# Performance work log

Measured on AMD Instinct MI355X. Metric: run time of the kernel, lower is better.

## Reference

```python
import jax, jax.numpy as jnp
import numpy as np

B, NMAX, D, NUM = 1024, 128, 256, 4
EPS = 1e-8
NEG = -1e9


def segment_softmax(logits, seg):
    # torch_geometric-style softmax over ragged segments. logits: (T,)
    m = jax.ops.segment_max(logits, seg, num_segments=B)
    e = jnp.exp(logits - m[seg])
    s = jax.ops.segment_sum(e, seg, num_segments=B)
    return e / (s[seg] + 1e-16)


def to_dense(v, seg, pos):
    # scatter ragged rows into (B, NMAX, ...) dense batch
    return jnp.zeros((B, NMAX) + v.shape[1:], v.dtype).at[seg, pos].set(v)


def uot_badmm(x, q0d, maskf, a1, a2, a3, rho):
    # Bregman-ADMM solver for entropic unbalanced OT (f_method='badmm-e').
    # x: (B,N,D) cost (to be maximized); q0d, maskf: (B,N,1); a1,a2,a3,rho: (NUM,)
    log_p0 = jnp.full((B, 1, D), -jnp.log(float(D)), x.dtype)  # uniform dim prior
    log_q0 = jnp.log(q0d + EPS)                                # (B,N,1)
    log_t = log_q0 + log_p0                                    # T init = q0 p0^T
    log_s = log_t
    log_mu = log_p0
    log_eta = log_q0
    z = jnp.zeros_like(x)
    z1 = jnp.zeros_like(log_p0)
    z2 = jnp.zeros_like(log_q0)
    neg = (1.0 - maskf) * NEG  # exclude padded rows from N-axis softmax
    for k in range(NUM):
        r, b1, b2, b3 = rho[k], a1[k], a2[k], a3[k]
        # T-update: rows (over D) sum to eta
        y = (x - z + r * log_s) / (b2 + r)
        log_t = log_eta + jax.nn.log_softmax(y, axis=2)
        # S-update: columns (over N) sum to mu, masked
        y = (z + r * log_t) / (b1 + r) + neg
        log_s = log_mu + jax.nn.log_softmax(y, axis=1)
        # unbalanced marginal updates (KL to priors, weight a3)
        log_mu = (b3 * log_p0 - z1 + r * jax.nn.logsumexp(log_s, axis=1, keepdims=True)) / (b3 + r)
        log_eta = (b3 * log_q0 - z2 + r * jax.nn.logsumexp(log_t, axis=2, keepdims=True)) / (b3 + r)
        # dual ascent
        t = jnp.exp(log_t) * maskf
        s = jnp.exp(log_s) * maskf
        z = z + r * (t - s)
        z1 = z1 + r * (jnp.exp(log_mu) - jnp.sum(s, axis=1, keepdims=True))
        z2 = z2 + r * (jnp.exp(log_eta) - jnp.sum(t, axis=2, keepdims=True)) * maskf
    return jnp.exp(log_t) * maskf


def setup_inputs() -> dict:
    rng = np.random.default_rng(0)
    lengths = rng.integers(NMAX // 2, NMAX + 1, size=B)
    lengths[0] = NMAX  # ensure max size present
    batch = jnp.asarray(np.repeat(np.arange(B), lengths), dtype=jnp.int32)
    total = int(lengths.sum())
    ks = jax.random.split(jax.random.key(0), 8)
    x = jax.random.normal(ks[0], (total, D), jnp.float32)
    W1 = jax.random.normal(ks[1], (2 * D, D), jnp.float32) / np.float32(np.sqrt(D))
    W2 = jax.random.normal(ks[2], (1, 2 * D), jnp.float32) / np.float32(np.sqrt(2 * D))
    rho = 0.1 * jax.random.normal(ks[3], (NUM,), jnp.float32)
    a1 = 0.1 * jax.random.normal(ks[4], (NUM,), jnp.float32)
    a2 = 0.1 * jax.random.normal(ks[5], (NUM,), jnp.float32)
    a3 = 0.1 * jax.random.normal(ks[6], (NUM,), jnp.float32)
    return {"x": x, "batch": batch, "W1": W1, "W2": W2, "rho": rho, "a1": a1, "a2": a2, "a3": a3}


def reference(x, batch, W1, W2, rho, a1, a2, a3):
    # attention-based sample prior q0 (q0 != 'fixed' branch)
    h = jnp.tanh(x @ W1.T)          # (T, 2D)
    logits = (h @ W2.T)[:, 0]       # (T,)
    q0 = segment_softmax(logits, batch)[:, None]  # (T, 1)
    # ragged -> dense batch (to_dense_batch)
    counts = jax.ops.segment_sum(jnp.ones_like(batch), batch, num_segments=B)
    starts = jnp.cumsum(counts) - counts
    pos = jnp.arange(batch.shape[0]) - starts[batch]
    xd = to_dense(x, batch, pos)    # (B, NMAX, D)
    q0d = to_dense(q0, batch, pos)  # (B, NMAX, 1)
    mask = to_dense(jnp.ones((batch.shape[0], 1), x.dtype), batch, pos)  # (B, NMAX, 1)
    trans = uot_badmm(xd, q0d, mask,
                      jax.nn.softplus(a1), jax.nn.softplus(a2),
                      jax.nn.softplus(a3), jax.nn.softplus(rho))
    frot = D * xd * trans * mask    # (B, NMAX, D)
    return jnp.sum(frot, axis=1)    # (B, D)
```

## Files before the change

### kernel.cpp

```cpp
#include <hip/hip_runtime.h>
#include <math.h>

#define BB   1024
#define DD   256
#define LOGD 5.5451774444795624753f

typedef __attribute__((ext_vector_type(8))) short short8;
typedef __attribute__((ext_vector_type(4))) float f32x4;

__device__ __forceinline__ float wave_sum(float v){
  #pragma unroll
  for (int off=32; off>0; off>>=1) v += __shfl_xor(v, off, 64);
  return v;
}
__device__ __forceinline__ float wave_max(float v){
  #pragma unroll
  for (int off=32; off>0; off>>=1) v = fmaxf(v, __shfl_xor(v, off, 64));
  return v;
}
__device__ __forceinline__ float fast_tanh(float x){
  return 1.0f - 2.0f/(__expf(2.0f*x)+1.0f);
}
__device__ __forceinline__ unsigned short f2bf(float f){
  unsigned int u = __float_as_uint(f);
  unsigned int r = u + 0x7FFFu + ((u >> 16) & 1u);
  return (unsigned short)(r >> 16);
}

__global__ void k_pre(const float* __restrict__ W1, unsigned short* __restrict__ w1b,
                      const int* __restrict__ batch, int T, int* __restrict__ starts,
                      const float* __restrict__ rho, const float* __restrict__ a1,
                      const float* __restrict__ a2, const float* __restrict__ a3,
                      float* __restrict__ P)
{
  const int blk = blockIdx.x, tid = threadIdx.x;
  if (blk < 64){
    const int t = blk*256 + tid;
    #pragma unroll
    for (int i=0;i<2;i++){
      const int idx = (t*2 + i)*4;
      const float4 v = *(const float4*)(W1 + idx);
      *(ushort4*)(w1b + idx) = make_ushort4(f2bf(v.x), f2bf(v.y), f2bf(v.z), f2bf(v.w));
    }
  } else if (blk < 69){
    const int b = (blk-64)*256 + tid;
    if (b <= BB){
      int lo = 0, hi = T;
      while (lo < hi){ int mid = (lo+hi)>>1; if (batch[mid] < b) lo = mid+1; else hi = mid; }
      starts[b] = lo;
    }
  } else if (tid == 0){
    float lm = -LOGD, z1 = 0.f;
    for (int k=0;k<4;k++){
      float r  = log1pf(expf(rho[k]));
      float b1 = log1pf(expf(a1[k]));
      float b2 = log1pf(expf(a2[k]));
      float b3 = log1pf(expf(a3[k]));
      P[k]    = r;
      P[4+k]  = 1.f/(b1+r);
      P[8+k]  = 1.f/(b2+r);
      P[12+k] = lm;
      P[16+k] = b3;
      P[20+k] = 1.f/(b3+r);
      float lmn = (b3*(-LOGD) - z1 + r*lm)/(b3+r);
      z1 += r*(expf(lmn)-expf(lm));
      lm = lmn;
    }
  }
}

#define LPW 72
__global__ __launch_bounds__(512, 2) void k_mlp(
    const float* __restrict__ x, const unsigned short* __restrict__ w1b,
    const float* __restrict__ W2, float* __restrict__ logits, int T)
{
  __shared__ unsigned short Xs[128*LPW];
  __shared__ unsigned short Ws[128*LPW];
  __shared__ float lred[128];
  const int by = blockIdx.x;
  const int bx = blockIdx.y;
  const int tid = threadIdx.x;
  if (tid < 128) lred[tid] = 0.f;

  const int l = tid & 63;
  const int w = tid >> 6;
  const int wm = w >> 2;
  const int wn = w & 3;
  const int lr = l & 15, quad = l >> 4;
  const int srow = tid >> 2;
  const int sseg = tid & 3;
  const int wrow = tid >> 3;
  const int wseg = tid & 7;

  f32x4 acc[4][2];
  #pragma unroll
  for (int mi=0;mi<4;mi++)
    #pragma unroll
    for (int ni=0;ni<2;ni++) acc[mi][ni] = (f32x4){0.f,0.f,0.f,0.f};

  for (int kt=0; kt<4; kt++){
    const int k0 = kt*64;
    {
      const int grow = bx*128 + srow;
      #pragma unroll
      for (int i=0;i<4;i++){
        float4 v = make_float4(0.f,0.f,0.f,0.f);
        if (grow < T) v = *(const float4*)(x + (size_t)grow*DD + k0 + sseg*16 + i*4);
        *(ushort4*)&Xs[srow*LPW + sseg*16 + i*4] =
            make_ushort4(f2bf(v.x), f2bf(v.y), f2bf(v.z), f2bf(v.w));
      }
    }
    #pragma unroll
    for (int h=0; h<2; h++){
      const int r = h*64 + wrow;
      *(short8*)&Ws[r*LPW + wseg*8] =
          *(const short8*)(w1b + (size_t)(by*128 + r)*DD + k0 + wseg*8);
    }
    __syncthreads();
    #pragma unroll
    for (int ks=0; ks<2; ks++){
      short8 afr[4], bfr[2];
      #pragma unroll
      for (int mi=0;mi<4;mi++)
        afr[mi] = *(const short8*)&Xs[(wm*64 + mi*16 + lr)*LPW + ks*32 + quad*8];
      #pragma unroll
      for (int ni=0;ni<2;ni++)
        bfr[ni] = *(const short8*)&Ws[(wn*32 + ni*16 + lr)*LPW + ks*32 + quad*8];
      #pragma unroll
      for (int mi=0;mi<4;mi++)
        #pragma unroll
        for (int ni=0;ni<2;ni++)
          acc[mi][ni] = __builtin_amdgcn_mfma_f32_16x16x32_bf16(afr[mi], bfr[ni], acc[mi][ni], 0, 0, 0);
    }
    __syncthreads();
  }

  float w2v[2];
  #pragma unroll
  for (int ni=0;ni<2;ni++) w2v[ni] = W2[by*128 + wn*32 + ni*16 + lr];
  #pragma unroll
  for (int mi=0;mi<4;mi++){
    float p[4];
    #pragma unroll
    for (int v=0; v<4; v++){
      p[v] = fast_tanh(acc[mi][0][v])*w2v[0] + fast_tanh(acc[mi][1][v])*w2v[1];
      #pragma unroll
      for (int off=1; off<16; off<<=1) p[v] += __shfl_xor(p[v], off, 64);
    }
    if (lr == 0){
      #pragma unroll
      for (int v=0; v<4; v++)
        atomicAdd(&lred[wm*64 + mi*16 + quad*4 + v], p[v]);
    }
  }
  __syncthreads();
  if (tid < 128){
    const int grow = bx*128 + tid;
    if (grow < T) atomicAdd(logits + grow, lred[tid]);
  }
}

__global__ __launch_bounds__(1024, 4) void k_solver(
    const float* __restrict__ x, const float* __restrict__ logits,
    const int* __restrict__ starts, const float* __restrict__ P,
    float* __restrict__ out)
{
  __shared__ float A[128*DD];
  __shared__ float red[16*DD];
  __shared__ float colv[DD];
  const int b = blockIdx.x;
  const int start = starts[b];
  const int len = starts[b+1] - start;
  const int tid = threadIdx.x;
  const int w = tid >> 6, l = tid & 63;
  const int n0 = w*8;
  int nv = len - n0; nv = nv < 0 ? 0 : (nv > 8 ? 8 : nv);

  const float r0=P[0], r1=P[1], r2=P[2], r3=P[3];
  const float i10=P[4], i11=P[5], i12=P[6];
  const float i20=P[8], i21=P[9], i22=P[10], i23=P[11];
  const float mu0=P[12], mu1=P[13], mu2=P[14];
  const float b30=P[16], b31=P[17], b32=P[18];
  const float e30=P[20], e31=P[21], e32=P[22];

  const float* lg = logits + start;
  float v0 = (l      < len) ? lg[l]    : -3.0e38f;
  float v1 = (l+64   < len) ? lg[l+64] : -3.0e38f;
  float sm = wave_max(fmaxf(v0,v1));
  float se0 = (l    < len) ? __expf(v0-sm) : 0.f;
  float se1 = (l+64 < len) ? __expf(v1-sm) : 0.f;
  float ssum = wave_sum(se0+se1);
  const float sinv = 1.f/(ssum + 1e-16f);
  const float esel = (n0 < 64) ? se0 : se1;

  float lq[8], eta[8], z2r[8];
  float z[8][4];
  #pragma unroll
  for (int r=0;r<8;r++){
    const float ev = __shfl(esel, (n0+r)&63, 64);
    lq[r]  = __logf(ev*sinv + 1e-8f);
    eta[r] = lq[r];
    z2r[r] = 0.f;
    #pragma unroll
    for (int j=0;j<4;j++) z[r][j]=0.f;
  }

  {
    float sp[4] = {0.f,0.f,0.f,0.f};
    #pragma unroll
    for (int r=0;r<8;r++){
      if (r < nv){
        const float* xp = x + (size_t)(start+n0+r)*DD + l;
        const int base = (n0+r)*DD + l;
        const float a0 = lq[r] - LOGD;
        float xv[4], y[4];
        #pragma unroll
        for (int j=0;j<4;j++) xv[j] = xp[64*j];
        #pragma unroll
        for (int j=0;j<4;j++) y[j] = (xv[j] + r0*a0) * i20;
        float se = 0.f;
        #pragma unroll
        for (int j=0;j<4;j++) se += __expf(y[j]);
        se = wave_sum(se);
        const float off = eta[r] - __logf(se);
        #pragma unroll
        for (int j=0;j<4;j++){
          const float lt = off + y[j];
          A[base+64*j] = lt;
          sp[j] += __expf((r0*lt) * i10);
        }
        const float en = (b30*lq[r] - z2r[r] + r0*eta[r]) * e30;
        z2r[r] += r0*(__expf(en) - __expf(eta[r]));
        eta[r] = en;
      }
    }
    #pragma unroll
    for (int j=0;j<4;j++) red[w*DD + l + 64*j] = sp[j];
  }
  __syncthreads();
  if (tid < DD){
    float s = 0.f;
    #pragma unroll
    for (int ww=0; ww<16; ww++) s += red[ww*DD + tid];
    colv[tid] = __logf(s);
  }
  __syncthreads();

  #pragma unroll
  for (int k=1;k<3;k++){
    const float rkm = (k==1)? r0 : r1;
    const float ib1m= (k==1)? i10 : i11;
    const float mum = (k==1)? mu0 : mu1;
    const float rk  = (k==1)? r1 : r2;
    const float ib1k= (k==1)? i11 : i12;
    const float ib2k= (k==1)? i21 : i22;
    const float b3k = (k==1)? b31 : b32;
    const float e3k = (k==1)? e31 : e32;
    float lsc[4];
    #pragma unroll
    for (int j=0;j<4;j++) lsc[j] = colv[l+64*j];
    float sp[4] = {0.f,0.f,0.f,0.f};
    #pragma unroll
    for (int r=0;r<8;r++){
      if (r < nv){
        const float* xp = x + (size_t)(start+n0+r)*DD + l;
        const int base = (n0+r)*DD + l;
        float xv[4];
        #pragma unroll
        for (int j=0;j<4;j++) xv[j] = xp[64*j];
        float y[4], lsn[4];
        #pragma unroll
        for (int j=0;j<4;j++){
          const float lt  = A[base+64*j];
          const float ys  = (z[r][j] + rkm*lt) * ib1m;
          lsn[j] = mum + ys - lsc[j];
          z[r][j] += rkm*(__expf(lt) - __expf(lsn[j]));
          y[j] = (xv[j] - z[r][j] + rk*lsn[j]) * ib2k;
        }
        float se = 0.f;
        #pragma unroll
        for (int j=0;j<4;j++) se += __expf(y[j]);
        se = wave_sum(se);
        const float off = eta[r] - __logf(se);
        #pragma unroll
        for (int j=0;j<4;j++){
          const float lt = off + y[j];
          A[base+64*j] = lt;
          sp[j] += __expf((z[r][j] + rk*lt) * ib1k);
        }
        const float en = (b3k*lq[r] - z2r[r] + rk*eta[r]) * e3k;
        z2r[r] += rk*(__expf(en) - __expf(eta[r]));
        eta[r] = en;
      }
    }
    #pragma unroll
    for (int j=0;j<4;j++) red[w*DD + l + 64*j] = sp[j];
    __syncthreads();
    if (tid < DD){
      float s = 0.f;
      #pragma unroll
      for (int ww=0; ww<16; ww++) s += red[ww*DD + tid];
      colv[tid] = __logf(s);
    }
    __syncthreads();
  }

  {
    float lsc[4];
    #pragma unroll
    for (int j=0;j<4;j++) lsc[j] = colv[l+64*j];
    float op[4] = {0.f,0.f,0.f,0.f};
    #pragma unroll
    for (int r=0;r<8;r++){
      if (r < nv){
        const float* xp = x + (size_t)(start+n0+r)*DD + l;
        const int base = (n0+r)*DD + l;
        float xv[4];
        #pragma unroll
        for (int j=0;j<4;j++) xv[j] = xp[64*j];
        float y[4];
        #pragma unroll
        for (int j=0;j<4;j++){
          const float lt  = A[base+64*j];
          const float ys  = (z[r][j] + r2*lt) * i12;
          const float lsn = mu2 + ys - lsc[j];
          z[r][j] += r2*(__expf(lt) - __expf(lsn));
          y[j] = (xv[j] - z[r][j] + r3*lsn) * i23;
        }
        float ey[4], se = 0.f;
        #pragma unroll
        for (int j=0;j<4;j++){ ey[j] = __expf(y[j]); se += ey[j]; }
        se = wave_sum(se);
        const float rs = __expf(eta[r]) / se;
        #pragma unroll
        for (int j=0;j<4;j++) op[j] += xv[j]*ey[j]*rs;
      }
    }
    #pragma unroll
    for (int j=0;j<4;j++) red[w*DD + l + 64*j] = op[j];
    __syncthreads();
    if (tid < DD){
      float s = 0.f;
      #pragma unroll
      for (int ww=0; ww<16; ww++) s += red[ww*DD + tid];
      out[(size_t)b*DD + tid] = 256.0f * s;
    }
  }
}

extern "C" void kernel_launch(void* const* d_in, const int* in_sizes, int n_in,
                              void* d_out, int out_size, void* d_ws, size_t ws_size,
                              hipStream_t stream) {
  const float* x    = (const float*)d_in[0];
  const int*   batch= (const int*)d_in[1];
  const float* W1   = (const float*)d_in[2];
  const float* W2   = (const float*)d_in[3];
  const float* rho  = (const float*)d_in[4];
  const float* a1   = (const float*)d_in[5];
  const float* a2   = (const float*)d_in[6];
  const float* a3   = (const float*)d_in[7];
  float* out = (float*)d_out;
  const int T = in_sizes[1];

  float* logits = (float*)d_ws;
  int*   starts = (int*)(logits + T);
  float* P      = (float*)(starts + 1028);
  unsigned short* w1b = (unsigned short*)(P + 32);

  k_pre<<<70, 256, 0, stream>>>(W1, w1b, batch, T, starts, rho, a1, a2, a3, P);
  hipMemsetAsync(logits, 0, (size_t)T*sizeof(float), stream);
  k_mlp<<<dim3(4, (T+127)/128), 512, 0, stream>>>(x, w1b, W2, logits, T);
  k_solver<<<BB, 1024, 0, stream>>>(x, logits, starts, P, out);
}
```

Before: 358.2 us.

## Keep full x tile resident in MLP, drop memset, use LDS atomics in solver

The MLP kernel now loads a row tile of x once into LDS as bf16 across the full K dimension and loops over all four hidden-column chunks inside one block. Logits are written directly instead of accumulated with global atomics, so the memset launch is removed. In the solver, the 16-way shared reduction buffer plus its extra barrier pass is replaced by LDS atomicAdd into a triple-buffered column array, which saves one barrier per iteration and some LDS. The cost is larger LDS use in k_mlp (about 135 KB per block, against 36 KB before), fewer and longer MLP blocks, and contention on the shared atomics.

Result: slower. 472.4 us (+31.9%).

```diff
diff --git a/kernel.cpp b/kernel.cpp
--- a/kernel.cpp
+++ b/kernel.cpp
@@ -69,94 +69,88 @@
   }
 }
 
-#define LPW 72
+#define LPX 264
 __global__ __launch_bounds__(512, 2) void k_mlp(
     const float* __restrict__ x, const unsigned short* __restrict__ w1b,
     const float* __restrict__ W2, float* __restrict__ logits, int T)
 {
-  __shared__ unsigned short Xs[128*LPW];
-  __shared__ unsigned short Ws[128*LPW];
+  __shared__ unsigned short Xs[128*LPX];
+  __shared__ unsigned short Ws[128*LPX];
   __shared__ float lred[128];
-  const int by = blockIdx.x;
-  const int bx = blockIdx.y;
+  const int bx = blockIdx.x;
   const int tid = threadIdx.x;
   if (tid < 128) lred[tid] = 0.f;
+
+  const int srow = tid >> 2, sseg = tid & 3;
+  {
+    const int grow = bx*128 + srow;
+    #pragma unroll
+    for (int i=0;i<16;i++){
+      float4 v = make_float4(0.f,0.f,0.f,0.f);
+      if (grow < T) v = *(const float4*)(x + (size_t)grow*DD + sseg*64 + i*4);
+      *(ushort4*)&Xs[srow*LPX + sseg*64 + i*4] =
+          make_ushort4(f2bf(v.x), f2bf(v.y), f2bf(v.z), f2bf(v.w));
+    }
+  }
 
   const int l = tid & 63;
   const int w = tid >> 6;
   const int wm = w >> 2;
   const int wn = w & 3;
   const int lr = l & 15, quad = l >> 4;
-  const int srow = tid >> 2;
-  const int sseg = tid & 3;
-  const int wrow = tid >> 3;
-  const int wseg = tid & 7;
-
-  f32x4 acc[4][2];
-  #pragma unroll
-  for (int mi=0;mi<4;mi++)
-    #pragma unroll
-    for (int ni=0;ni<2;ni++) acc[mi][ni] = (f32x4){0.f,0.f,0.f,0.f};
-
-  for (int kt=0; kt<4; kt++){
-    const int k0 = kt*64;
-    {
-      const int grow = bx*128 + srow;
-      #pragma unroll
-      for (int i=0;i<4;i++){
-        float4 v = make_float4(0.f,0.f,0.f,0.f);
-        if (grow < T) v = *(const float4*)(x + (size_t)grow*DD + k0 + sseg*16 + i*4);
-        *(ushort4*)&Xs[srow*LPW + sseg*16 + i*4] =
-            make_ushort4(f2bf(v.x), f2bf(v.y), f2bf(v.z), f2bf(v.w));
-      }
-    }
-    #pragma unroll
-    for (int h=0; h<2; h++){
-      const int r = h*64 + wrow;
-      *(short8*)&Ws[r*LPW + wseg*8] =
-          *(const short8*)(w1b + (size_t)(by*128 + r)*DD + k0 + wseg*8);
-    }
+
+  for (int hq=0; hq<4; hq++){
     __syncthreads();
     #pragma unroll
-    for (int ks=0; ks<2; ks++){
+    for (int i=0;i<8;i++){
+      *(short8*)&Ws[srow*LPX + sseg*64 + i*8] =
+          *(const short8*)(w1b + (size_t)(hq*128 + srow)*DD + sseg*64 + i*8);
+    }
+    __syncthreads();
+
+    f32x4 acc[4][2];
+    #pragma unroll
+    for (int mi=0;mi<4;mi++)
+      #pragma unroll
+      for (int ni=0;ni<2;ni++) acc[mi][ni] = (f32x4){0.f,0.f,0.f,0.f};
+    #pragma unroll
+    for (int ks=0; ks<8; ks++){
       short8 afr[4], bfr[2];
       #pragma unroll
       for (int mi=0;mi<4;mi++)
-        afr[mi] = *(const short8*)&Xs[(wm*64 + mi*16 + lr)*LPW + ks*32 + quad*8];
+        afr[mi] = *(const short8*)&Xs[(wm*64 + mi*16 + lr)*LPX + ks*32 + quad*8];
       #pragma unroll
       for (int ni=0;ni<2;ni++)
-        bfr[ni] = *(const short8*)&Ws[(wn*32 + ni*16 + lr)*LPW + ks*32 + quad*8];
+        bfr[ni] = *(const short8*)&Ws[(wn*32 + ni*16 + lr)*LPX + ks*32 + quad*8];
       #pragma unroll
       for (int mi=0;mi<4;mi++)
         #pragma unroll
         for (int ni=0;ni<2;ni++)
           acc[mi][ni] = __builtin_amdgcn_mfma_f32_16x16x32_bf16(afr[mi], bfr[ni], acc[mi][ni], 0, 0, 0);
     }
-    __syncthreads();
-  }
-
-  float w2v[2];
-  #pragma unroll
-  for (int ni=0;ni<2;ni++) w2v[ni] = W2[by*128 + wn*32 + ni*16 + lr];
-  #pragma unroll
-  for (int mi=0;mi<4;mi++){
-    float p[4];
-    #pragma unroll
-    for (int v=0; v<4; v++){
-      p[v] = fast_tanh(acc[mi][0][v])*w2v[0] + fast_tanh(acc[mi][1][v])*w2v[1];
-      #pragma unroll
-      for (int off=1; off<16; off<<=1) p[v] += __shfl_xor(p[v], off, 64);
-    }
-    if (lr == 0){
-      #pragma unroll
-      for (int v=0; v<4; v++)
-        atomicAdd(&lred[wm*64 + mi*16 + quad*4 + v], p[v]);
+    float w2v[2];
+    #pragma unroll
+    for (int ni=0;ni<2;ni++) w2v[ni] = W2[hq*128 + wn*32 + ni*16 + lr];
+    #pragma unroll
+    for (int mi=0;mi<4;mi++){
+      float p[4];
+      #pragma unroll
+      for (int v=0; v<4; v++){
+        p[v] = fast_tanh(acc[mi][0][v])*w2v[0] + fast_tanh(acc[mi][1][v])*w2v[1];
+        #pragma unroll
+        for (int off=1; off<16; off<<=1) p[v] += __shfl_xor(p[v], off, 64);
+      }
+      if (lr == 0){
+        #pragma unroll
+        for (int v=0; v<4; v++)
+          atomicAdd(&lred[wm*64 + mi*16 + quad*4 + v], p[v]);
+      }
     }
   }
   __syncthreads();
   if (tid < 128){
     const int grow = bx*128 + tid;
-    if (grow < T) atomicAdd(logits + grow, lred[tid]);
+    if (grow < T) logits[grow] = lred[tid];
   }
 }
 
@@ -166,8 +160,7 @@
     float* __restrict__ out)
 {
   __shared__ float A[128*DD];
-  __shared__ float red[16*DD];
-  __shared__ float colv[DD];
+  __shared__ float cols[3][DD];
   const int b = blockIdx.x;
   const int start = starts[b];
   const int len = starts[b+1] - start;
@@ -204,6 +197,8 @@
     #pragma unroll
     for (int j=0;j<4;j++) z[r][j]=0.f;
   }
+  if (tid < DD){ cols[0][tid] = 0.f; cols[1][tid] = 0.f; }
+  __syncthreads();
 
   {
     float sp[4] = {0.f,0.f,0.f,0.f};
@@ -234,15 +229,10 @@
         eta[r] = en;
       }
     }
-    #pragma unroll
-    for (int j=0;j<4;j++) red[w*DD + l + 64*j] = sp[j];
-  }
-  __syncthreads();
-  if (tid < DD){
-    float s = 0.f;
-    #pragma unroll
-    for (int ww=0; ww<16; ww++) s += red[ww*DD + tid];
-    colv[tid] = __logf(s);
+    if (nv > 0){
+      #pragma unroll
+      for (int j=0;j<4;j++) atomicAdd(&cols[0][l+64*j], sp[j]);
+    }
   }
   __syncthreads();
 
@@ -256,9 +246,11 @@
     const float ib2k= (k==1)? i21 : i22;
     const float b3k = (k==1)? b31 : b32;
     const float e3k = (k==1)? e31 : e32;
+    const int pm = (k-1)%3, pc = k%3, pz = (k+1)%3;
     float lsc[4];
     #pragma unroll
-    for (int j=0;j<4;j++) lsc[j] = colv[l+64*j];
+    for (int j=0;j<4;j++) lsc[j] = __logf(cols[pm][l+64*j]);
+    if (tid < DD) cols[pz][tid] = 0.f;
     float sp[4] = {0.f,0.f,0.f,0.f};
     #pragma unroll
     for (int r=0;r<8;r++){
@@ -293,14 +285,9 @@
         eta[r] = en;
       }
     }
-    #pragma unroll
-    for (int j=0;j<4;j++) red[w*DD + l + 64*j] = sp[j];
-    __syncthreads();
-    if (tid < DD){
-      float s = 0.f;
-      #pragma unroll
-      for (int ww=0; ww<16; ww++) s += red[ww*DD + tid];
-      colv[tid] = __logf(s);
+    if (nv > 0){
+      #pragma unroll
+      for (int j=0;j<4;j++) atomicAdd(&cols[pc][l+64*j], sp[j]);
     }
     __syncthreads();
   }
@@ -308,7 +295,7 @@
   {
     float lsc[4];
     #pragma unroll
-    for (int j=0;j<4;j++) lsc[j] = colv[l+64*j];
+    for (int j=0;j<4;j++) lsc[j] = __logf(cols[2][l+64*j]);
     float op[4] = {0.f,0.f,0.f,0.f};
     #pragma unroll
     for (int r=0;r<8;r++){
@@ -336,15 +323,12 @@
         for (int j=0;j<4;j++) op[j] += xv[j]*ey[j]*rs;
       }
     }
-    #pragma unroll
-    for (int j=0;j<4;j++) red[w*DD + l + 64*j] = op[j];
+    if (nv > 0){
+      #pragma unroll
+      for (int j=0;j<4;j++) atomicAdd(&cols[0][l+64*j], op[j]);
+    }
     __syncthreads();
-    if (tid < DD){
-      float s = 0.f;
-      #pragma unroll
-      for (int ww=0; ww<16; ww++) s += red[ww*DD + tid];
-      out[(size_t)b*DD + tid] = 256.0f * s;
-    }
+    if (tid < DD) out[(size_t)b*DD + tid] = 256.0f * cols[0][tid];
   }
 }
 
@@ -368,7 +352,6 @@
   unsigned short* w1b = (unsigned short*)(P + 32);
 
   k_pre<<<70, 256, 0, stream>>>(W1, w1b, batch, T, starts, rho, a1, a2, a3, P);
-  hipMemsetAsync(logits, 0, (size_t)T*sizeof(float), stream);
-  k_mlp<<<dim3(4, (T+127)/128), 512, 0, stream>>>(x, w1b, W2, logits, T);
+  k_mlp<<<dim3((T+127)/128), 512, 0, stream>>>(x, w1b, W2, logits, T);
   k_solver<<<BB, 1024, 0, stream>>>(x, logits, starts, P, out);
 }
```
